# Optimization experiments

Measured on AMD Instinct MI355X. Metric: run time of the kernel, lower is better.

Reference implementation:

```python
import jax, jax.numpy as jnp
import numpy as np

B, T, C = 4, 1024, 1024
H, KV, D = 16, 8, 64   # n_head, kv_heads, dim_head
L = 32                 # partial rotary dim (freqs.shape[-1])
QK_NORM_SCALE = 10.0


def l2norm(t):
    # F.normalize(t, dim=-1): divide by L2 norm clamped to eps
    n = jnp.linalg.norm(t, axis=-1, keepdims=True)
    return t / jnp.maximum(n, 1e-12)


def rotate_half(x):
    # lucidrains rotary: interleaved pairs (d r) with r=2 -> (-x2, x1)
    x1, x2 = x[..., 0::2], x[..., 1::2]
    return jnp.stack((-x2, x1), axis=-1).reshape(x.shape)


def apply_rope(t, freqs):
    # xpos_scale is None in this config -> scale = 1.0
    return t * jnp.cos(freqs) + rotate_half(t) * jnp.sin(freqs)


def setup_inputs() -> dict:
    key = jax.random.key(0)
    ks = jax.random.split(key, 10)
    x = jax.random.normal(ks[0], (B, T, C), dtype=jnp.float32)
    encoded_data = jax.random.normal(ks[1], (B, T, C), dtype=jnp.float32)
    # rotary freqs: positions x inverse frequencies, duplicated interleaved to length L
    pos = jnp.arange(T, dtype=jnp.float32)
    inv_freq = 10000.0 ** (-jnp.arange(L // 2, dtype=jnp.float32) / (L // 2))
    freqs = jnp.repeat(pos[:, None] * inv_freq[None, :], 2, axis=-1)  # (T, L)
    attn_bias = jax.random.normal(ks[2], (H, T, T), dtype=jnp.float32) * 0.02
    Wq = jax.random.normal(ks[3], (C, H * D), dtype=jnp.float32) * 0.02
    Wk = jax.random.normal(ks[4], (C, KV * D), dtype=jnp.float32) * 0.02
    Wv = jax.random.normal(ks[5], (C, KV * D), dtype=jnp.float32) * 0.02
    Wo = jax.random.normal(ks[6], (H * D, C), dtype=jnp.float32) * 0.02
    q_scale = jnp.ones((D,), dtype=jnp.float32)
    k_scale = jnp.ones((D,), dtype=jnp.float32)
    return {"x": x, "encoded_data": encoded_data, "freqs": freqs,
            "attn_bias": attn_bias, "Wq": Wq, "Wk": Wk, "Wv": Wv, "Wo": Wo,
            "q_scale": q_scale, "k_scale": k_scale}


def reference(x, encoded_data, freqs, attn_bias, Wq, Wk, Wv, Wo, q_scale, k_scale):
    Bx, Tx, Cx = x.shape
    q = (x @ Wq).reshape(Bx, Tx, H, D).transpose(0, 2, 1, 3)            # (B,H,T,D)
    k = (encoded_data @ Wk).reshape(Bx, Tx, KV, D).transpose(0, 2, 1, 3)  # (B,KV,T,D)
    v = (encoded_data @ Wv).reshape(Bx, Tx, KV, D).transpose(0, 2, 1, 3)

    # qk-norm
    q = l2norm(q) * q_scale
    k = l2norm(k) * k_scale

    # partial rotary on first L dims (v too, as in the original code)
    l = freqs.shape[-1]
    ql, qr = q[..., :l], q[..., l:]
    kl, kr = k[..., :l], k[..., l:]
    vl, vr = v[..., :l], v[..., l:]
    q = jnp.concatenate([apply_rope(ql, freqs), qr], axis=-1)
    k = jnp.concatenate([apply_rope(kl, freqs), kr], axis=-1)
    v = jnp.concatenate([apply_rope(vl, freqs), vr], axis=-1)

    # GQA: k,v repeated along head dim (KV -> H = 2*KV)
    k = jnp.tile(k, (1, 2, 1, 1))
    v = jnp.tile(v, (1, 2, 1, 1))

    # pre-scale q, then SDPA applies its own default D^-0.5 (faithful to source)
    default_scale = D ** (-0.5)
    q = q * (default_scale / QK_NORM_SCALE)

    mask_value = -jnp.finfo(q.dtype).max
    causal = jnp.triu(jnp.ones((Tx, Tx), dtype=bool), k=1)  # j > i masked
    bias = jnp.where(causal, mask_value / 2, attn_bias)      # (H,T,T)

    scores = jnp.einsum('bhqd,bhkd->bhqk', q, k) * default_scale + bias[None]
    attn = jax.nn.softmax(scores, axis=-1)
    y = jnp.einsum('bhqk,bhkd->bhqd', attn, v)                # (B,H,T,D)
    y = y.transpose(0, 2, 1, 3).reshape(Bx, Tx, H * D)
    return y @ Wo
```

## Files before the change

### kernel.cpp

```cpp
#include <hip/hip_runtime.h>

typedef unsigned short u16;
typedef __attribute__((ext_vector_type(8))) __bf16 bf16x8;
typedef __attribute__((ext_vector_type(4))) float f32x4;
typedef __attribute__((ext_vector_type(16))) float f32x16;

#define LOG2E 1.44269504088896f

__device__ __forceinline__ u16 f2bf(float f) {
  union { float f; unsigned u; } c; c.f = f;
  unsigned u = c.u;
  return (u16)((u + 0x7fffu + ((u >> 16) & 1u)) >> 16);
}
__device__ __forceinline__ float bf2f(u16 h) {
  union { unsigned u; float f; } c; c.u = ((unsigned)h) << 16;
  return c.f;
}

__device__ __forceinline__ void load_lds16(const void* g, void* l) {
  __builtin_amdgcn_global_load_lds((const __attribute__((address_space(1))) unsigned int*)g,
                                   (__attribute__((address_space(3))) unsigned int*)l, 16, 0, 0);
}

__global__ void prologue_kernel(const float* __restrict__ x, const float* __restrict__ enc,
                                const float* __restrict__ freqs,
                                const float* __restrict__ Wq, const float* __restrict__ Wk,
                                const float* __restrict__ Wv, const float* __restrict__ Wo,
                                u16* __restrict__ xb, u16* __restrict__ eb,
                                u16* __restrict__ WqT, u16* __restrict__ WkT,
                                u16* __restrict__ WvT, u16* __restrict__ WoT,
                                float* __restrict__ cstab, float* __restrict__ sntab) {
  __shared__ float tile[32][33];
  int id = blockIdx.x;
  int tid = threadIdx.x;
  if (id < 2048) {
    const int n4each = 1048576;
    int stride = 2048 * 256;
    for (int i = id * 256 + tid; i < 2 * n4each; i += stride) {
      const float4* src; ushort4* dst; int j;
      if (i < n4each) { src = (const float4*)x; dst = (ushort4*)xb; j = i; }
      else            { src = (const float4*)enc; dst = (ushort4*)eb; j = i - n4each; }
      float4 v = src[j];
      ushort4 o;
      o.x = f2bf(v.x); o.y = f2bf(v.y); o.z = f2bf(v.z); o.w = f2bf(v.w);
      dst[j] = o;
    }
    return;
  }
  if (id < 2176) {
    int i = (id - 2048) * 256 + tid;
    float f = freqs[i];
    float sn, cs;
    sincosf(f, &sn, &cs);
    cstab[i] = cs; sntab[i] = sn;
    return;
  }
  int rem = id - 2176;
  int z = rem >> 10;
  int ry = (rem >> 5) & 31;
  int rx = rem & 31;
  const float* in; u16* out; int C;
  if (z == 0)      { in = Wq; out = WqT; C = 1024; }
  else if (z == 1) { in = Wk; out = WkT; C = 512; }
  else if (z == 2) { in = Wv; out = WvT; C = 512; }
  else             { in = Wo; out = WoT; C = 1024; }
  const int R = 1024;
  int c0 = rx * 32, r0 = ry * 32;
  if (c0 >= C) return;
  int tx = tid & 31, ty = tid >> 5;
#pragma unroll
  for (int i = 0; i < 4; ++i)
    tile[ty + 8 * i][tx] = in[(size_t)(r0 + ty + 8 * i) * C + c0 + tx];
  __syncthreads();
#pragma unroll
  for (int i = 0; i < 4; ++i)
    out[(size_t)(c0 + ty + 8 * i) * R + r0 + tx] = f2bf(tile[tx][ty + 8 * i]);
}

__device__ __forceinline__ void gemm_bn64_dbuf(const u16* A, const u16* Bt, int K,
                                               char* sh, int m0, int n0, f32x4 (&acc)[2][4]) {
  int tid = threadIdx.x;
  int w = tid >> 6, l = tid & 63;
  int g = l >> 4, lr = l & 15;
#pragma unroll
  for (int m = 0; m < 2; ++m)
#pragma unroll
    for (int n = 0; n < 4; ++n) acc[m][n] = (f32x4){0.f, 0.f, 0.f, 0.f};

  auto stage = [&](int buf, int k0) {
    char* As = sh + buf * 24576;
    char* Bs = As + 16384;
#pragma unroll
    for (int rnd = 0; rnd < 4; ++rnd) {
      int bidx = rnd * 4096 + w * 1024 + l * 16;
      int row = bidx >> 7, colb = bidx & 127;
      int scol = colb ^ ((row & 7) << 4);
      load_lds16((const char*)A + ((size_t)(m0 + row) * K + k0) * 2 + scol,
                 As + rnd * 4096 + w * 1024);
    }
#pragma unroll
    for (int rnd = 0; rnd < 2; ++rnd) {
      int bidx = rnd * 4096 + w * 1024 + l * 16;
      int row = bidx >> 7, colb = bidx & 127;
      int scol = colb ^ ((row & 7) << 4);
      load_lds16((const char*)Bt + ((size_t)(n0 + row) * K + k0) * 2 + scol,
                 Bs + rnd * 4096 + w * 1024);
    }
  };

  stage(0, 0);
  __syncthreads();
  int nk = K >> 6;
  for (int ki = 0; ki < nk; ++ki) {
    int cur = ki & 1;
    if (ki + 1 < nk) stage(cur ^ 1, (ki + 1) << 6);
    const char* As = sh + cur * 24576;
    const char* Bs = As + 16384;
    bf16x8 af[2][2], bfr[4][2];
#pragma unroll
    for (int m = 0; m < 2; ++m) {
      int ra = w * 32 + m * 16 + lr;
#pragma unroll
      for (int kf = 0; kf < 2; ++kf)
        af[m][kf] = *(const bf16x8*)(As + ra * 128 + ((kf * 64 + g * 16) ^ ((ra & 7) << 4)));
    }
#pragma unroll
    for (int n = 0; n < 4; ++n) {
      int rb = n * 16 + lr;
#pragma unroll
      for (int kf = 0; kf < 2; ++kf)
        bfr[n][kf] = *(const bf16x8*)(Bs + rb * 128 + ((kf * 64 + g * 16) ^ ((rb & 7) << 4)));
    }
#pragma unroll
    for (int m = 0; m < 2; ++m)
#pragma unroll
      for (int n = 0; n < 4; ++n) {
        acc[m][n] = __builtin_amdgcn_mfma_f32_16x16x32_bf16(af[m][0], bfr[n][0], acc[m][n], 0, 0, 0);
        acc[m][n] = __builtin_amdgcn_mfma_f32_16x16x32_bf16(af[m][1], bfr[n][1], acc[m][n], 0, 0, 0);
      }
    __syncthreads();
  }
}

__global__ __launch_bounds__(256, 3) void gemm_qkv_kernel(const u16* xb, const u16* eb,
                                                          const u16* WqT, const u16* WkT, const u16* WvT,
                                                          const float* __restrict__ qscale,
                                                          const float* __restrict__ kscale,
                                                          const float* __restrict__ cstab,
                                                          const float* __restrict__ sntab,
                                                          const float* __restrict__ bias,
                                                          u16* Qb, u16* Ktiles, u16* Vtiles,
                                                          u16* __restrict__ biasTT) {
  __shared__ __align__(16) char sh[49152];
  int id = blockIdx.x;
  int sel = id % 3;
  if (sel == 2) {
    int flat = id / 3;
    int w = threadIdx.x >> 6, lane = threadIdx.x & 63;
    float* lt = (float*)(sh + w * 4224);
    int ql = lane & 31, hi = lane >> 5;
    for (int f = flat * 4 + w; f < 8448; f += 2048) {
      int h = f / 528, rem = f - h * 528;
      int qt = (int)((sqrtf(8.f * (float)rem + 1.f) - 1.f) * 0.5f);
      while ((qt + 1) * (qt + 2) / 2 <= rem) ++qt;
      while (qt * (qt + 1) / 2 > rem) --qt;
      int kt = rem - qt * (qt + 1) / 2;
      const float* tsrc = bias + ((size_t)h * 1024 + qt * 32) * 1024 + kt * 32;
#pragma unroll
      for (int i = 0; i < 4; ++i) {
        int row = i * 8 + (lane >> 3);
        int c4 = (lane & 7) * 4;
        float4 v4 = *(const float4*)(tsrc + (size_t)row * 1024 + c4);
        lt[row * 33 + c4 + 0] = v4.x; lt[row * 33 + c4 + 1] = v4.y;
        lt[row * 33 + c4 + 2] = v4.z; lt[row * 33 + c4 + 3] = v4.w;
      }
      u16 v[16];
#pragma unroll
      for (int r = 0; r < 16; ++r) {
        int c = (r & 3) + 8 * (r >> 2) + 4 * hi;
        v[r] = f2bf(lt[ql * 33 + c] * LOG2E);
      }
      u16* dst = biasTT + (size_t)f * 1024 + lane * 16;
#pragma unroll
      for (int i = 0; i < 4; ++i) {
        ushort4 o; o.x = v[i * 4]; o.y = v[i * 4 + 1]; o.z = v[i * 4 + 2]; o.w = v[i * 4 + 3];
        *(ushort4*)(dst + i * 4) = o;
      }
    }
    return;
  }
  int gi = (id / 3) * 2 + sel;
  int xblk = gi & 31;
  int t = gi >> 5;
  int z, y;
  if (t < 16)      { z = 0; y = t; }
  else if (t < 24) { z = 1; y = t - 16; }
  else             { z = 2; y = t - 24; }
  const u16* A; const u16* Bt;
  if (z == 0)      { A = xb; Bt = WqT; }
  else if (z == 1) { A = eb; Bt = WkT; }
  else             { A = eb; Bt = WvT; }
  int m0 = xblk * 128, n0 = y * 64;

  f32x4 acc[2][4];
  gemm_bn64_dbuf(A, Bt, 1024, sh, m0, n0, acc);

  int tid = threadIdx.x;
  int w = tid >> 6, l = tid & 63;
  int g = l >> 4, lr = l & 15;
  int head = n0 >> 6;

  if (z == 2) {
#pragma unroll
    for (int m = 0; m < 2; ++m) {
      int rowb = m0 + w * 32 + m * 16 + g * 4;
#pragma unroll
      for (int r = 0; r < 4; ++r) {
        int row = rowb + r;
        int t2 = row & 1023, b = row >> 10;
        char* tbase = (char*)Vtiles + (size_t)((b * 8 + head) * 32 + (t2 >> 5)) * 4096;
        int kb = (t2 & 31) * 2;
#pragma unroll
        for (int n = 0; n < 4; ++n) {
          int dloc = n * 16 + lr;
          float v = acc[m][n][r];
          if (n < 2) {
            float cs = cstab[t2 * 32 + dloc];
            float sn = sntab[t2 * 32 + dloc];
            float partner = __shfl_xor(v, 1);
            float rot = (lr & 1) ? partner : -partner;
            v = v * cs + rot * sn;
          }
          int rr = dloc & 31;
          int scol = ((dloc >> 5) << 6) | kb;
          *(u16*)(tbase + rr * 128 + (scol ^ ((rr & 7) << 4))) = f2bf(v);
        }
      }
    }
    return;
  }

  const float* scale = (z == 0) ? qscale : kscale;
  float fs = (z == 0) ? 0.0015625f * LOG2E : 1.0f;
#pragma unroll
  for (int m = 0; m < 2; ++m) {
    int rowb = m0 + w * 32 + m * 16 + g * 4;
#pragma unroll
    for (int r = 0; r < 4; ++r) {
      int row = rowb + r;
      int t2 = row & 1023, b = row >> 10;
      float ss = 0.f;
#pragma unroll
      for (int n = 0; n < 4; ++n) { float v = acc[m][n][r]; ss += v * v; }
#pragma unroll
      for (int d = 1; d < 16; d <<= 1) ss += __shfl_xor(ss, d);
      float inv = 1.0f / fmaxf(sqrtf(ss), 1e-12f);
#pragma unroll
      for (int n = 0; n < 4; ++n) {
        int dloc = n * 16 + lr;
        float v = acc[m][n][r] * inv * scale[dloc];
        if (n < 2) {
          float cs = cstab[t2 * 32 + dloc];
          float sn = sntab[t2 * 32 + dloc];
          float partner = __shfl_xor(v, 1);
          float rot = (lr & 1) ? partner : -partner;
          v = v * cs + rot * sn;
        }
        v *= fs;
        if (z == 0) {
          Qb[((size_t)(b * 16 + head) * 1024 + t2) * 64 + dloc] = f2bf(v);
        } else {
          int tile = (b * 8 + head) * 32 + (t2 >> 5);
          int rin = t2 & 31;
          *(u16*)((char*)Ktiles + (size_t)tile * 4096 + rin * 128 + ((dloc * 2) ^ ((rin & 7) << 4))) = f2bf(v);
        }
      }
    }
  }
}

__global__ __launch_bounds__(256, 3) void gemm_out_kernel(const u16* Yb, const u16* WoT, float* out) {
  __shared__ __align__(16) char sh[49152];
  int id = blockIdx.x;
  int m0 = (id & 31) * 128, n0 = (id >> 5) * 64;
  f32x4 acc[2][4];
  gemm_bn64_dbuf(Yb, WoT, 1024, sh, m0, n0, acc);
  int tid = threadIdx.x;
  int w = tid >> 6, l = tid & 63;
  int g = l >> 4, lr = l & 15;
#pragma unroll
  for (int m = 0; m < 2; ++m)
#pragma unroll
    for (int n = 0; n < 4; ++n) {
      int row = m0 + w * 32 + m * 16 + g * 4;
      int col = n0 + n * 16 + lr;
#pragma unroll
      for (int r = 0; r < 4; ++r)
        out[(size_t)(row + r) * 1024 + col] = acc[m][n][r];
    }
}

__device__ __forceinline__ unsigned pack_bf2(float lo, float hi_) {
  union { __bf16 h[2]; unsigned u; } c;
  c.h[0] = (__bf16)lo; c.h[1] = (__bf16)hi_;
  return c.u;
}

__global__ __launch_bounds__(256, 4) void attn_kernel(const u16* __restrict__ Qb, const u16* __restrict__ Ktiles,
                                                      const u16* __restrict__ Vtiles, const u16* __restrict__ biasTT,
                                                      u16* __restrict__ Yb) {
  __shared__ __align__(16) char smem[33280];
  int tid = threadIdx.x;
  int w = tid >> 6;
  int lane = tid & 63;
  int ql = lane & 31;
  int hi = lane >> 5;
  int id = blockIdx.x;
  int xcd = id & 7;
  int j = id >> 3;
  int b = j & 3;
  int gslot = j >> 2;
  int g = gslot * 8 + xcd;
  int h = g & 15;
  int qt = 31 - (g >> 4);
  int kv = h & 7;
  int qg = qt * 32 + ql;
  int nt = qt + 1;

  char* stg = smem + w * 8192;

  const u16* Qrow = Qb + ((size_t)(b * 16 + h) * 1024 + qg) * 64;
  bf16x8 qf[4];
#pragma unroll
  for (int ks = 0; ks < 4; ++ks) qf[ks] = *(const bf16x8*)(Qrow + ks * 16 + hi * 8);

  const char* Ktb = (const char*)Ktiles + (size_t)((b * 8 + kv) * 32) * 4096;
  const char* Vtb = (const char*)Vtiles + (size_t)((b * 8 + kv) * 32) * 4096;
  const u16* btb = biasTT + (size_t)(h * 528 + qt * (qt + 1) / 2) * 1024;

  f32x16 o0, o1;
#pragma unroll
  for (int r = 0; r < 16; ++r) { o0[r] = 0.f; o1[r] = 0.f; }
  float lsum = 0.f;

  for (int it = w; it < nt; it += 4) {
    int t0 = it * 32;
    const char* Ksrc = Ktb + (size_t)it * 4096 + lane * 16;
    const char* Vsrc = Vtb + (size_t)it * 4096 + lane * 16;
#pragma unroll
    for (int i = 0; i < 4; ++i) load_lds16(Ksrc + i * 1024, stg + i * 1024);
#pragma unroll
    for (int i = 0; i < 4; ++i) load_lds16(Vsrc + i * 1024, stg + 4096 + i * 1024);
    __builtin_amdgcn_sched_barrier(0);
    asm volatile("s_waitcnt vmcnt(4)" ::: "memory");
    __builtin_amdgcn_sched_barrier(0);
    const u16* bl = btb + (size_t)it * 1024 + lane * 16;
    bf16x8 ba = *(const bf16x8*)bl;
    bf16x8 bb2 = *(const bf16x8*)(bl + 8);
    f32x16 s;
#pragma unroll
    for (int r = 0; r < 16; ++r) s[r] = 0.f;
#pragma unroll
    for (int ks = 0; ks < 4; ++ks) {
      bf16x8 kc = *(const bf16x8*)(stg + ql * 128 + ((ks * 32 + hi * 16) ^ ((ql & 7) << 4)));
      s = __builtin_amdgcn_mfma_f32_32x32x16_bf16(kc, qf[ks], s, 0, 0, 0);
    }
    bool diag = (it == nt - 1);
    float p[16];
    float ssum = 0.f;
#pragma unroll
    for (int r = 0; r < 16; ++r) {
      float sv = s[r] + (float)(r < 8 ? ba[r & 7] : bb2[r & 7]);
      if (diag) {
        int key = t0 + (r & 3) + 8 * (r >> 2) + 4 * hi;
        if (key > qg) sv = -1e30f;
      }
      float pe = exp2f(sv);
      p[r] = pe;
      ssum += pe;
    }
    lsum += ssum;
    unsigned pk[8], tk[8];
#pragma unroll
    for (int j2 = 0; j2 < 8; ++j2) pk[j2] = pack_bf2(p[2 * j2], p[2 * j2 + 1]);
#pragma unroll
    for (int j2 = 0; j2 < 8; ++j2) tk[j2] = (unsigned)__shfl_xor((int)pk[j2], 32);
    union PU { unsigned u[4]; bf16x8 v; };
    PU pb0, pb1;
    pb0.u[0] = hi ? tk[2] : pk[0];
    pb0.u[1] = hi ? tk[3] : pk[1];
    pb0.u[2] = hi ? pk[2] : tk[0];
    pb0.u[3] = hi ? pk[3] : tk[1];
    pb1.u[0] = hi ? tk[6] : pk[4];
    pb1.u[1] = hi ? tk[7] : pk[5];
    pb1.u[2] = hi ? pk[6] : tk[4];
    pb1.u[3] = hi ? pk[7] : tk[5];
    asm volatile("s_waitcnt vmcnt(0)" ::: "memory");
    __builtin_amdgcn_sched_barrier(0);
    char* Vl = stg + 4096;
    bf16x8 v00 = *(const bf16x8*)(Vl + ql * 128 + (((0 << 6) | (0 * 32 + hi * 16)) ^ ((ql & 7) << 4)));
    bf16x8 v01 = *(const bf16x8*)(Vl + ql * 128 + (((0 << 6) | (1 * 32 + hi * 16)) ^ ((ql & 7) << 4)));
    bf16x8 v10 = *(const bf16x8*)(Vl + ql * 128 + (((1 << 6) | (0 * 32 + hi * 16)) ^ ((ql & 7) << 4)));
    bf16x8 v11 = *(const bf16x8*)(Vl + ql * 128 + (((1 << 6) | (1 * 32 + hi * 16)) ^ ((ql & 7) << 4)));
    o0 = __builtin_amdgcn_mfma_f32_32x32x16_bf16(v00, pb0.v, o0, 0, 0, 0);
    o0 = __builtin_amdgcn_mfma_f32_32x32x16_bf16(v01, pb1.v, o0, 0, 0, 0);
    o1 = __builtin_amdgcn_mfma_f32_32x32x16_bf16(v10, pb0.v, o1, 0, 0, 0);
    o1 = __builtin_amdgcn_mfma_f32_32x32x16_bf16(v11, pb1.v, o1, 0, 0, 0);
  }

  lsum += __shfl_xor(lsum, 32);
  u16* Osh = (u16*)stg;
  float* Lsh = (float*)(smem + 32768);
#pragma unroll
  for (int r = 0; r < 16; ++r) {
    int row = (r & 3) + 8 * (r >> 2) + 4 * hi;
    Osh[row * 32 + ql]        = f2bf(o0[r]);
    Osh[(row + 32) * 32 + ql] = f2bf(o1[r]);
  }
  if (hi == 0) Lsh[w * 32 + ql] = lsum;
  __syncthreads();

  {
    int q = tid & 31, dg = tid >> 5;
    float* Lsh2 = (float*)(smem + 32768);
    float ltot = Lsh2[q] + Lsh2[32 + q] + Lsh2[64 + q] + Lsh2[96 + q];
    float invl = 1.0f / ltot;
    u16 ov[8];
#pragma unroll
    for (int j2 = 0; j2 < 8; ++j2) {
      int d = dg * 8 + j2;
      float acc = bf2f(*(u16*)(smem + 0 * 8192 + (d * 32 + q) * 2)) +
                  bf2f(*(u16*)(smem + 1 * 8192 + (d * 32 + q) * 2)) +
                  bf2f(*(u16*)(smem + 2 * 8192 + (d * 32 + q) * 2)) +
                  bf2f(*(u16*)(smem + 3 * 8192 + (d * 32 + q) * 2));
      ov[j2] = f2bf(acc * invl);
    }
    ushort4 out0, out1;
    out0.x = ov[0]; out0.y = ov[1]; out0.z = ov[2]; out0.w = ov[3];
    out1.x = ov[4]; out1.y = ov[5]; out1.z = ov[6]; out1.w = ov[7];
    u16* Yp = Yb + ((size_t)b * 1024 + qt * 32 + q) * 1024 + h * 64 + dg * 8;
    *(ushort4*)Yp = out0;
    *(ushort4*)(Yp + 4) = out1;
  }
}

extern "C" void kernel_launch(void* const* d_in, const int* in_sizes, int n_in,
                              void* d_out, int out_size, void* d_ws, size_t ws_size,
                              hipStream_t stream) {
  const float* x     = (const float*)d_in[0];
  const float* enc   = (const float*)d_in[1];
  const float* freqs = (const float*)d_in[2];
  const float* bias  = (const float*)d_in[3];
  const float* Wq    = (const float*)d_in[4];
  const float* Wk    = (const float*)d_in[5];
  const float* Wv    = (const float*)d_in[6];
  const float* Wo    = (const float*)d_in[7];
  const float* qs    = (const float*)d_in[8];
  const float* ks    = (const float*)d_in[9];

  char* ws = (char*)d_ws;
  size_t off = 0;
  auto alloc = [&](size_t bytes) { char* p = ws + off; off += (bytes + 255) & ~(size_t)255; return p; };
  u16*   xb     = (u16*)alloc(8388608);
  u16*   eb     = (u16*)alloc(8388608);
  u16*   WqT    = (u16*)alloc(2097152);
  u16*   WkT    = (u16*)alloc(1048576);
  u16*   WvT    = (u16*)alloc(1048576);
  u16*   WoT    = (u16*)alloc(2097152);
  u16*   Qb     = (u16*)alloc(8388608);
  u16*   Ktiles = (u16*)alloc(4194304);
  u16*   Vtiles = (u16*)alloc(4194304);
  u16*   biasTT = (u16*)alloc(17301504);
  float* cstab  = (float*)alloc(131072);
  float* sntab  = (float*)alloc(131072);
  u16*   Yb     = (u16*)xb;

  prologue_kernel<<<6272, 256, 0, stream>>>(x, enc, freqs, Wq, Wk, Wv, Wo,
                                            xb, eb, WqT, WkT, WvT, WoT, cstab, sntab);

  gemm_qkv_kernel<<<1536, 256, 0, stream>>>(xb, eb, WqT, WkT, WvT,
                                            qs, ks, cstab, sntab, bias,
                                            Qb, Ktiles, Vtiles, biasTT);

  attn_kernel<<<dim3(2048), 256, 0, stream>>>(Qb, Ktiles, Vtiles, biasTT, Yb);

  gemm_out_kernel<<<512, 256, 0, stream>>>(Yb, WoT, (float*)d_out);
}
```

Before: 92.60 us.

## Single-buffer GEMM LDS staging to raise occupancy and reorder tile mapping

Replaces the double-buffered LDS staging in the shared GEMM helper with a single buffer that loads, syncs, computes and syncs again. This halves LDS per block (48KB to 24KB), and launch bounds rise from 3 to 4 blocks per SM for both the QKV and output GEMM kernels. The block-to-tile mapping is also swapped so that consecutive blocks walk along N for the same M rows, which may improve L2 reuse of the A operand. The trade-off is losing the overlap of the next tile's global-to-LDS load with the current tile's MFMAs, relying on more resident waves to hide latency instead.

```diff
diff --git a/kernel.cpp b/kernel.cpp
--- a/kernel.cpp
+++ b/kernel.cpp
@@ -77,8 +77,9 @@
     out[(size_t)(c0 + ty + 8 * i) * R + r0 + tx] = f2bf(tile[tx][ty + 8 * i]);
 }
 
-__device__ __forceinline__ void gemm_bn64_dbuf(const u16* A, const u16* Bt, int K,
-                                               char* sh, int m0, int n0, f32x4 (&acc)[2][4]) {
+__device__ __forceinline__ void gemm_bn64_core(const u16* A, const u16* Bt, int K,
+                                               u16* As, u16* Bs, int m0, int n0,
+                                               f32x4 (&acc)[2][4]) {
   int tid = threadIdx.x;
   int w = tid >> 6, l = tid & 63;
   int g = l >> 4, lr = l & 15;
@@ -87,16 +88,14 @@
 #pragma unroll
     for (int n = 0; n < 4; ++n) acc[m][n] = (f32x4){0.f, 0.f, 0.f, 0.f};
 
-  auto stage = [&](int buf, int k0) {
-    char* As = sh + buf * 24576;
-    char* Bs = As + 16384;
+  for (int k0 = 0; k0 < K; k0 += 64) {
 #pragma unroll
     for (int rnd = 0; rnd < 4; ++rnd) {
       int bidx = rnd * 4096 + w * 1024 + l * 16;
       int row = bidx >> 7, colb = bidx & 127;
       int scol = colb ^ ((row & 7) << 4);
       load_lds16((const char*)A + ((size_t)(m0 + row) * K + k0) * 2 + scol,
-                 As + rnd * 4096 + w * 1024);
+                 (char*)As + rnd * 4096 + w * 1024);
     }
 #pragma unroll
     for (int rnd = 0; rnd < 2; ++rnd) {
@@ -104,32 +103,23 @@
       int row = bidx >> 7, colb = bidx & 127;
       int scol = colb ^ ((row & 7) << 4);
       load_lds16((const char*)Bt + ((size_t)(n0 + row) * K + k0) * 2 + scol,
-                 Bs + rnd * 4096 + w * 1024);
-    }
-  };
-
-  stage(0, 0);
-  __syncthreads();
-  int nk = K >> 6;
-  for (int ki = 0; ki < nk; ++ki) {
-    int cur = ki & 1;
-    if (ki + 1 < nk) stage(cur ^ 1, (ki + 1) << 6);
-    const char* As = sh + cur * 24576;
-    const char* Bs = As + 16384;
+                 (char*)Bs + rnd * 4096 + w * 1024);
+    }
+    __syncthreads();
     bf16x8 af[2][2], bfr[4][2];
 #pragma unroll
     for (int m = 0; m < 2; ++m) {
       int ra = w * 32 + m * 16 + lr;
 #pragma unroll
       for (int kf = 0; kf < 2; ++kf)
-        af[m][kf] = *(const bf16x8*)(As + ra * 128 + ((kf * 64 + g * 16) ^ ((ra & 7) << 4)));
+        af[m][kf] = *(const bf16x8*)((const char*)As + ra * 128 + ((kf * 64 + g * 16) ^ ((ra & 7) << 4)));
     }
 #pragma unroll
     for (int n = 0; n < 4; ++n) {
       int rb = n * 16 + lr;
 #pragma unroll
       for (int kf = 0; kf < 2; ++kf)
-        bfr[n][kf] = *(const bf16x8*)(Bs + rb * 128 + ((kf * 64 + g * 16) ^ ((rb & 7) << 4)));
+        bfr[n][kf] = *(const bf16x8*)((const char*)Bs + rb * 128 + ((kf * 64 + g * 16) ^ ((rb & 7) << 4)));
     }
 #pragma unroll
     for (int m = 0; m < 2; ++m)
@@ -142,7 +132,7 @@
   }
 }
 
-__global__ __launch_bounds__(256, 3) void gemm_qkv_kernel(const u16* xb, const u16* eb,
+__global__ __launch_bounds__(256, 4) void gemm_qkv_kernel(const u16* xb, const u16* eb,
                                                           const u16* WqT, const u16* WkT, const u16* WvT,
                                                           const float* __restrict__ qscale,
                                                           const float* __restrict__ kscale,
@@ -151,7 +141,9 @@
                                                           const float* __restrict__ bias,
                                                           u16* Qb, u16* Ktiles, u16* Vtiles,
                                                           u16* __restrict__ biasTT) {
-  __shared__ __align__(16) char sh[49152];
+  __shared__ __align__(16) char sh[24576];
+  u16* As = (u16*)sh;
+  u16* Bs = (u16*)(sh + 16384);
   int id = blockIdx.x;
   int sel = id % 3;
   if (sel == 2) {
@@ -190,8 +182,8 @@
     return;
   }
   int gi = (id / 3) * 2 + sel;
-  int xblk = gi & 31;
-  int t = gi >> 5;
+  int xblk = gi >> 5;
+  int t = gi & 31;
   int z, y;
   if (t < 16)      { z = 0; y = t; }
   else if (t < 24) { z = 1; y = t - 16; }
@@ -203,7 +195,7 @@
   int m0 = xblk * 128, n0 = y * 64;
 
   f32x4 acc[2][4];
-  gemm_bn64_dbuf(A, Bt, 1024, sh, m0, n0, acc);
+  gemm_bn64_core(A, Bt, 1024, As, Bs, m0, n0, acc);
 
   int tid = threadIdx.x;
   int w = tid >> 6, l = tid & 63;
@@ -279,12 +271,13 @@
   }
 }
 
-__global__ __launch_bounds__(256, 3) void gemm_out_kernel(const u16* Yb, const u16* WoT, float* out) {
-  __shared__ __align__(16) char sh[49152];
+__global__ __launch_bounds__(256, 4) void gemm_out_kernel(const u16* Yb, const u16* WoT, float* out) {
+  __shared__ __align__(16) u16 As[128 * 64];
+  __shared__ __align__(16) u16 Bs[64 * 64];
   int id = blockIdx.x;
-  int m0 = (id & 31) * 128, n0 = (id >> 5) * 64;
+  int m0 = (id >> 4) * 128, n0 = (id & 15) * 64;
   f32x4 acc[2][4];
-  gemm_bn64_dbuf(Yb, WoT, 1024, sh, m0, n0, acc);
+  gemm_bn64_core(Yb, WoT, 1024, As, Bs, m0, n0, acc);
   int tid = threadIdx.x;
   int w = tid >> 6, l = tid & 63;
   int g = l >> 4, lr = l & 15;
```

Result: slower. 105.8 us (+14.3%).
